# Kernel optimization log

Hardware: AMD Instinct MI355X
Metric: run time of the kernel (lower is better)

## Reference

```python
import jax, jax.numpy as jnp
import numpy as np

L = 4096          # total packed length
HID = 2560        # hidden_size
H = 8             # num_attention_heads
KV = 4            # num_key_value_heads
HD = 256          # head_dim
SW = 1024         # sliding_window
SCALING = 256.0 ** -0.5  # query_pre_attn_scalar ** -0.5
EPS = 1e-6
ROPE_BASE = 10000.0


def setup_inputs() -> dict:
    key = jax.random.key(0)
    ks = jax.random.split(key, 9)
    hidden_states = jax.random.normal(ks[0], (L, HID), jnp.float32)
    Wq = jax.random.normal(ks[1], (HID, H * HD), jnp.float32) * 0.02
    Wk = jax.random.normal(ks[2], (HID, KV * HD), jnp.float32) * 0.02
    Wv = jax.random.normal(ks[3], (HID, KV * HD), jnp.float32) * 0.02
    Wo = jax.random.normal(ks[4], (H * HD, HID), jnp.float32) * 0.02
    q_norm_w = jax.random.normal(ks[5], (HD,), jnp.float32) * 0.1
    k_norm_w = jax.random.normal(ks[6], (HD,), jnp.float32) * 0.1
    # 4 packed sequences of length 1024 each; positions restart per sequence
    cu_seqlens = jnp.array([0, 1024, 2048, 3072, 4096], jnp.int32)
    pos = jnp.tile(jnp.arange(1024, dtype=jnp.float32), 4)  # [L]
    inv_freq = 1.0 / (ROPE_BASE ** (jnp.arange(0, HD, 2, dtype=jnp.float32) / HD))
    freqs = pos[:, None] * inv_freq[None, :]                # [L, HD/2]
    emb = jnp.concatenate([freqs, freqs], axis=-1)          # [L, HD]
    cos, sin = jnp.cos(emb), jnp.sin(emb)
    return {"hidden_states": hidden_states, "cos": cos, "sin": sin,
            "Wq": Wq, "Wk": Wk, "Wv": Wv, "Wo": Wo,
            "q_norm_w": q_norm_w, "k_norm_w": k_norm_w,
            "cu_seqlens": cu_seqlens}


def _rotate_half(x):
    x1, x2 = x[..., : HD // 2], x[..., HD // 2:]
    return jnp.concatenate([-x2, x1], axis=-1)


def _rms_norm(x, w):
    # Gemma3RMSNorm: x * rsqrt(mean(x^2) + eps) * (1 + w)
    x32 = x.astype(jnp.float32)
    out = x32 * jax.lax.rsqrt(jnp.mean(x32 * x32, axis=-1, keepdims=True) + EPS)
    return (out * (1.0 + w.astype(jnp.float32))).astype(x.dtype)


def _packed_sliding_causal_mask(cu_seqlens, total_len):
    pos = jnp.arange(total_len)
    seq_ids = jnp.searchsorted(cu_seqlens[1:], pos, side='right')
    seq_mask = seq_ids[:, None] == seq_ids[None, :]
    dist = pos[None, :] - pos[:, None]                      # pos[j] - pos[i]
    causal = dist <= 0
    window = dist >= -(SW - 1)                              # left_window = SW - 1
    keep = seq_mask & causal & window
    return jnp.where(keep, 0.0, -jnp.inf).astype(jnp.float32)  # [L, L]


def reference(hidden_states, cos, sin, Wq, Wk, Wv, Wo, q_norm_w, k_norm_w, cu_seqlens):
    total_len = hidden_states.shape[0]
    # projections -> [n_heads, L, head_dim]
    q = (hidden_states @ Wq).reshape(total_len, H, HD).transpose(1, 0, 2)
    k = (hidden_states @ Wk).reshape(total_len, KV, HD).transpose(1, 0, 2)
    v = (hidden_states @ Wv).reshape(total_len, KV, HD).transpose(1, 0, 2)
    q = _rms_norm(q, q_norm_w)
    k = _rms_norm(k, k_norm_w)
    # RoPE (cos/sin broadcast over heads)
    q = q * cos + _rotate_half(q) * sin
    k = k * cos + _rotate_half(k) * sin
    # GQA repeat_kv: [KV, L, HD] -> [H, L, HD]
    n_rep = H // KV
    k = jnp.repeat(k, n_rep, axis=0)
    v = jnp.repeat(v, n_rep, axis=0)
    mask = _packed_sliding_causal_mask(cu_seqlens, total_len)
    scores = jnp.einsum('hqd,hkd->hqk', q, k) * SCALING + mask[None]
    attn = jax.nn.softmax(scores.astype(jnp.float32), axis=-1).astype(q.dtype)
    out = jnp.einsum('hqk,hkd->qhd', attn, v).reshape(total_len, H * HD)
    return out @ Wo  # [L, hidden]
```

## Files before the change

kernel.cpp:

```cpp
#include <hip/hip_runtime.h>
#include <hip/hip_bf16.h>

typedef unsigned short u16;
typedef float f32x4 __attribute__((ext_vector_type(4)));
typedef short bf16x8 __attribute__((ext_vector_type(8)));

__device__ __forceinline__ float bf2f(u16 u) {
    union { float f; unsigned int i; } c; c.i = ((unsigned int)u) << 16; return c.f;
}
__device__ __forceinline__ u16 f2bf(float f) {
    union { float f; unsigned int i; } c; c.f = f;
    unsigned int r = c.i + 0x7fffu + ((c.i >> 16) & 1u);
    return (u16)(r >> 16);
}
__device__ __forceinline__ void gload16(const void* g, void* l) {
    __builtin_amdgcn_global_load_lds(
        (const __attribute__((address_space(1))) void*)g,
        (__attribute__((address_space(3))) void*)l, 16, 0, 0);
}

__global__ __launch_bounds__(256) void convert_f32_bf16(
    const float* __restrict__ in, u16* __restrict__ out, int n8)
{
    int i = blockIdx.x * 256 + threadIdx.x;
    if (i >= n8) return;
    const float4 a = *(const float4*)&in[i * 8];
    const float4 b = *(const float4*)&in[i * 8 + 4];
    bf16x8 o;
    o[0] = (short)f2bf(a.x); o[1] = (short)f2bf(a.y);
    o[2] = (short)f2bf(a.z); o[3] = (short)f2bf(a.w);
    o[4] = (short)f2bf(b.x); o[5] = (short)f2bf(b.y);
    o[6] = (short)f2bf(b.z); o[7] = (short)f2bf(b.w);
    *(bf16x8*)&out[i * 8] = o;
}

__global__ __launch_bounds__(256) void transpose_f32_bf16(
    const float* __restrict__ in, u16* __restrict__ out, int R, int C)
{
    __shared__ u16 tile[32][34];
    const int tx = threadIdx.x & 31;
    const int ty = threadIdx.x >> 5;
    const size_t r0 = (size_t)blockIdx.y * 32;
    const size_t c0 = (size_t)blockIdx.x * 32;
#pragma unroll
    for (int i = 0; i < 4; ++i) {
        int r = ty + 8 * i;
        tile[r][tx] = f2bf(in[(r0 + r) * C + c0 + tx]);
    }
    __syncthreads();
#pragma unroll
    for (int i = 0; i < 4; ++i) {
        int r = ty + 8 * i;
        out[(c0 + r) * R + r0 + tx] = tile[tx][r];
    }
}

__global__ __launch_bounds__(256) void transpose_bf16(
    const u16* __restrict__ in, u16* __restrict__ out, int ldin, int ldout)
{
    __shared__ u16 tile[32][34];
    const int tx = threadIdx.x & 31;
    const int ty = threadIdx.x >> 5;
    const size_t r0 = (size_t)blockIdx.y * 32;
    const size_t c0 = (size_t)blockIdx.x * 32;
#pragma unroll
    for (int i = 0; i < 4; ++i) {
        int r = ty + 8 * i;
        tile[r][tx] = in[(r0 + r) * (size_t)ldin + c0 + tx];
    }
    __syncthreads();
#pragma unroll
    for (int i = 0; i < 4; ++i) {
        int r = ty + 8 * i;
        out[(c0 + r) * (size_t)ldout + r0 + tx] = tile[tx][r];
    }
}

template<typename TOUT>
__global__ __launch_bounds__(512, 2) void gemm_bt8p(
    const u16* __restrict__ A, const u16* __restrict__ Bt, TOUT* __restrict__ C,
    int M, int N, int K)
{
    __shared__ u16 As[2][2][128 * 64];
    __shared__ u16 Bs[2][2][128 * 64];
    const int tid  = threadIdx.x;
    const int lane = tid & 63;
    const int w    = tid >> 6;
    const int wm   = w >> 2;
    const int wn   = w & 3;
    const int g    = lane >> 4, c = lane & 15;

    const int nbx = gridDim.x;
    int lin = blockIdx.y * nbx + blockIdx.x;
    const int cpx = (nbx * gridDim.y) >> 3;
    lin = (lin & 7) * cpx + (lin >> 3);
    const size_t mbase = (size_t)(lin / nbx) * 256;
    const size_t nbase = (size_t)(lin % nbx) * 256;

    const int schunk = w * 2;
    const int srow0  = lane >> 3;
    const int sslot  = lane & 7;

    auto stageA = [&](int t, int half) {
        u16* dst = &As[t & 1][half][0];
        const u16* src = A + (mbase + half * 128) * (size_t)K + t * 64;
#pragma unroll
        for (int i = 0; i < 2; ++i) {
            const int ch = schunk + i;
            const int rw = ch * 8 + srow0;
            gload16(src + (size_t)rw * K + ((sslot ^ (rw & 7)) << 3), dst + ch * 512);
        }
    };
    auto stageB = [&](int t, int half) {
        u16* dst = &Bs[t & 1][half][0];
        const u16* src = Bt + (nbase + half * 128) * (size_t)K + t * 64;
#pragma unroll
        for (int i = 0; i < 2; ++i) {
            const int ch = schunk + i;
            const int rw = ch * 8 + srow0;
            gload16(src + (size_t)rw * K + ((sslot ^ (rw & 7)) << 3), dst + ch * 512);
        }
    };
    auto ldA = [&](int t, int m, int kk) -> bf16x8 {
        const int r = m * 16 + c;
        return *(const bf16x8*)&As[t & 1][wm][r * 64 + ((kk * 32 + g * 8) ^ ((r & 7) << 3))];
    };
    auto ldB = [&](int t, int n, int kk) -> bf16x8 {
        const int r = (wn & 1) * 64 + n * 16 + c;
        return *(const bf16x8*)&Bs[t & 1][wn >> 1][r * 64 + ((kk * 32 + g * 8) ^ ((r & 7) << 3))];
    };

    f32x4 acc[8][4];
#pragma unroll
    for (int m = 0; m < 8; ++m)
#pragma unroll
        for (int n = 0; n < 4; ++n) { acc[m][n][0]=0.f; acc[m][n][1]=0.f; acc[m][n][2]=0.f; acc[m][n][3]=0.f; }

    const int nT = K >> 6;

    stageA(0, 0); stageA(0, 1); stageB(0, 0); stageB(0, 1);
    asm volatile("s_waitcnt vmcnt(0)" ::: "memory");
    __builtin_amdgcn_sched_barrier(0);
    __builtin_amdgcn_s_barrier();

    for (int t = 0; t < nT; ++t) {
        bf16x8 bF[4][2], aF[2][2];
        const bool more = (t + 1 < nT);

#pragma unroll
        for (int n = 0; n < 4; ++n) { bF[n][0] = ldB(t, n, 0); bF[n][1] = ldB(t, n, 1); }
#pragma unroll
        for (int i = 0; i < 2; ++i) { aF[i][0] = ldA(t, i, 0); aF[i][1] = ldA(t, i, 1); }
        if (more) { stageA(t + 1, 0); stageA(t + 1, 1); }
        __builtin_amdgcn_s_barrier();
        __builtin_amdgcn_s_setprio(1);
#pragma unroll
        for (int kk = 0; kk < 2; ++kk)
#pragma unroll
            for (int i = 0; i < 2; ++i)
#pragma unroll
                for (int n = 0; n < 4; ++n)
                    acc[i][n] = __builtin_amdgcn_mfma_f32_16x16x32_bf16(
                        aF[i][kk], bF[n][kk], acc[i][n], 0, 0, 0);
        __builtin_amdgcn_s_setprio(0);
        __builtin_amdgcn_s_barrier();

#pragma unroll
        for (int q = 1; q < 4; ++q) {
#pragma unroll
            for (int i = 0; i < 2; ++i) { aF[i][0] = ldA(t, 2*q + i, 0); aF[i][1] = ldA(t, 2*q + i, 1); }
            if (q == 1 && more) { stageB(t + 1, 0); stageB(t + 1, 1); }
            __builtin_amdgcn_s_barrier();
            __builtin_amdgcn_s_setprio(1);
#pragma unroll
            for (int kk = 0; kk < 2; ++kk)
#pragma unroll
                for (int i = 0; i < 2; ++i)
#pragma unroll
                    for (int n = 0; n < 4; ++n)
                        acc[2*q + i][n] = __builtin_amdgcn_mfma_f32_16x16x32_bf16(
                            aF[i][kk], bF[n][kk], acc[2*q + i][n], 0, 0, 0);
            __builtin_amdgcn_s_setprio(0);
            __builtin_amdgcn_s_barrier();
        }

        asm volatile("s_waitcnt vmcnt(0)" ::: "memory");
        __builtin_amdgcn_sched_barrier(0);
        __builtin_amdgcn_s_barrier();
    }

#pragma unroll
    for (int m = 0; m < 8; ++m)
#pragma unroll
        for (int n = 0; n < 4; ++n)
#pragma unroll
            for (int i = 0; i < 4; ++i) {
                size_t r   = mbase + wm * 128 + m * 16 + g * 4 + i;
                size_t col = nbase + wn * 64 + n * 16 + c;
                if constexpr (sizeof(TOUT) == 4) C[r * (size_t)N + col] = acc[m][n][i];
                else                             C[r * (size_t)N + col] = f2bf(acc[m][n][i]);
            }
}

__global__ __launch_bounds__(256) void rmsnorm_rope(
    u16* __restrict__ buf, int ld, const float* __restrict__ wgt,
    const float* __restrict__ cosb, const float* __restrict__ sinb,
    int heads, float outscale)
{
    const int lane = threadIdx.x & 63;
    const int wv   = threadIdx.x >> 6;
    const int rid  = blockIdx.x * 4 + wv;
    const int t    = rid / heads;
    const int h    = rid - t * heads;
    u16* p = buf + (size_t)t * ld + h * 256 + lane * 4;

    ushort4 xu = *(const ushort4*)p;
    float x0 = bf2f(xu.x), x1 = bf2f(xu.y), x2 = bf2f(xu.z), x3 = bf2f(xu.w);
    float ss = x0*x0 + x1*x1 + x2*x2 + x3*x3;
#pragma unroll
    for (int msk = 1; msk < 64; msk <<= 1) ss += __shfl_xor(ss, msk);
    const float rstd = rsqrtf(ss * (1.0f / 256.0f) + 1e-6f);

    const int d0 = lane * 4;
    const float4 wv4 = *(const float4*)&wgt[d0];
    float xn0 = x0 * rstd * (1.0f + wv4.x);
    float xn1 = x1 * rstd * (1.0f + wv4.y);
    float xn2 = x2 * rstd * (1.0f + wv4.z);
    float xn3 = x3 * rstd * (1.0f + wv4.w);

    float pn0 = __shfl_xor(xn0, 32);
    float pn1 = __shfl_xor(xn1, 32);
    float pn2 = __shfl_xor(xn2, 32);
    float pn3 = __shfl_xor(xn3, 32);
    const float sgn = (lane < 32) ? -1.0f : 1.0f;

    const float4 cv = *(const float4*)&cosb[(size_t)t * 256 + d0];
    const float4 sv = *(const float4*)&sinb[(size_t)t * 256 + d0];
    float r0 = (xn0 * cv.x + sgn * pn0 * sv.x) * outscale;
    float r1 = (xn1 * cv.y + sgn * pn1 * sv.y) * outscale;
    float r2 = (xn2 * cv.z + sgn * pn2 * sv.z) * outscale;
    float r3 = (xn3 * cv.w + sgn * pn3 * sv.w) * outscale;

    ushort4 ou;
    ou.x = f2bf(r0); ou.y = f2bf(r1); ou.z = f2bf(r2); ou.w = f2bf(r3);
    *(ushort4*)p = ou;
}

__global__ __launch_bounds__(512, 2) void attn_kernel(
    const u16* __restrict__ q, int ldq,
    const u16* __restrict__ k, int ldk,
    const u16* __restrict__ vT,
    u16* __restrict__ Opart,
    float* __restrict__ stats)
{
    __shared__ u16 Ks[2][32 * 256];
    __shared__ u16 Vs[256 * 40];
    __shared__ u16 P[8][16][56];
    __shared__ float corrsF[8][16];
    const int tid  = threadIdx.x;
    const int lane = tid & 63;
    const int w    = tid >> 6;
    const int g    = lane >> 4, c = lane & 15;
    const int qt   = 15 - blockIdx.x;
    const int s    = blockIdx.y;
    const int kvh  = blockIdx.z & 3;
    const int kvs  = blockIdx.z >> 2;
    const int h    = kvh * 2 + (w >> 2);
    const int seq0 = s << 10;
    const int qrow0 = qt * 64 + (w & 3) * 16;
    const float NEG = -3.0e38f;

    bf16x8 qf[8];
    {
        const u16* qp = q + (size_t)(seq0 + qrow0 + c) * ldq + h * 256 + g * 8;
#pragma unroll
        for (int ch = 0; ch < 8; ++ch) qf[ch] = *(const bf16x8*)(qp + ch * 32);
    }

    const int kchunk0  = w * 2;
    const int krow_in  = (lane >> 5);
    const int kcol_lin = (lane & 31) * 16;
    const u16* kbase = k + (size_t)seq0 * ldk + kvh * 256;
    const int vd  = tid & 255;
    const int vj0 = (tid >> 8) * 2;
    const int vsw = (vd >> 3) & 3;
    const u16* vbase = vT + ((size_t)kvh * 256 + vd) * 4096 + seq0 + vj0 * 8;

    f32x4 oacc[16];
#pragma unroll
    for (int dt = 0; dt < 16; ++dt) { oacc[dt][0]=0.f; oacc[dt][1]=0.f; oacc[dt][2]=0.f; oacc[dt][3]=0.f; }
    float mq = -1e30f;
    float lq = 0.f;

    const int nt = qt + 1;
    const int t0 = kvs * nt;

    bf16x8 vreg[2];
#pragma unroll
    for (int i = 0; i < 2; ++i) {
        const int chunk = kchunk0 + i;
        const int row   = chunk * 2 + krow_in;
        const int bcol  = kcol_lin ^ ((row & 7) << 4);
        gload16(kbase + (size_t)(t0 * 32 + row) * ldk + (bcol >> 1), &Ks[0][chunk * 512]);
    }
#pragma unroll
    for (int j = 0; j < 2; ++j) vreg[j] = *(const bf16x8*)(vbase + t0 * 32 + j * 8);
    __syncthreads();
#pragma unroll
    for (int j = 0; j < 2; ++j)
        *(bf16x8*)&Vs[vd * 40 + (((vj0 + j) ^ vsw) * 8)] = vreg[j];
    __syncthreads();

    for (int ti = 0; ti < nt; ++ti) {
        const int p   = ti & 1;
        const int kv0 = (t0 + ti) * 32;

        if (ti + 1 < nt) {
#pragma unroll
            for (int i = 0; i < 2; ++i) {
                const int chunk = kchunk0 + i;
                const int row   = chunk * 2 + krow_in;
                const int bcol  = kcol_lin ^ ((row & 7) << 4);
                gload16(kbase + (size_t)(kv0 + 32 + row) * ldk + (bcol >> 1),
                        &Ks[p ^ 1][chunk * 512]);
            }
#pragma unroll
            for (int j = 0; j < 2; ++j) vreg[j] = *(const bf16x8*)(vbase + kv0 + 32 + j * 8);
        }

        f32x4 sacc[2];
#pragma unroll
        for (int nh = 0; nh < 2; ++nh) { sacc[nh][0]=0.f; sacc[nh][1]=0.f; sacc[nh][2]=0.f; sacc[nh][3]=0.f; }
        __builtin_amdgcn_s_setprio(1);
#pragma unroll
        for (int nh = 0; nh < 2; ++nh) {
            const int krow = nh * 16 + c;
#pragma unroll
            for (int ch = 0; ch < 8; ++ch) {
                const int sw = ((ch * 64 + g * 16) ^ ((c & 7) << 4)) >> 1;
                bf16x8 kf = *(const bf16x8*)&Ks[p][krow * 256 + sw];
                sacc[nh] = __builtin_amdgcn_mfma_f32_16x16x32_bf16(kf, qf[ch], sacc[nh], 0, 0, 0);
            }
        }
        __builtin_amdgcn_s_setprio(0);

        const int qloc = qrow0 + c;
        float pmax = NEG;
#pragma unroll
        for (int nh = 0; nh < 2; ++nh)
#pragma unroll
            for (int i = 0; i < 4; ++i) {
                if (kv0 + nh * 16 + g * 4 + i > qloc) sacc[nh][i] = NEG;
                pmax = fmaxf(pmax, sacc[nh][i]);
            }
        pmax = fmaxf(pmax, __shfl_xor(pmax, 16));
        pmax = fmaxf(pmax, __shfl_xor(pmax, 32));

        const bool rescale = !__all(pmax - mq <= 8.0f);
        float corr = 1.0f;
        if (rescale) {
            const float mn = fmaxf(mq, pmax);
            corr = __expf(mq - mn);
            mq = mn;
            if (g == 0) corrsF[w][c] = corr;
        }

        float rowsum = 0.f;
        unsigned int pw[4];
#pragma unroll
        for (int nh = 0; nh < 2; ++nh) {
            float p0 = __expf(sacc[nh][0] - mq);
            float p1 = __expf(sacc[nh][1] - mq);
            float p2 = __expf(sacc[nh][2] - mq);
            float p3 = __expf(sacc[nh][3] - mq);
            rowsum += (p0 + p1) + (p2 + p3);
            pw[nh * 2 + 0] = (unsigned int)f2bf(p0) | ((unsigned int)f2bf(p1) << 16);
            pw[nh * 2 + 1] = (unsigned int)f2bf(p2) | ((unsigned int)f2bf(p3) << 16);
        }
#pragma unroll
        for (int nh = 0; nh < 2; ++nh) {
            *(unsigned int*)&P[w][c][nh * 16 + g * 4]     = pw[nh * 2 + 0];
            *(unsigned int*)&P[w][c][nh * 16 + g * 4 + 2] = pw[nh * 2 + 1];
        }
        rowsum += __shfl_xor(rowsum, 16);
        rowsum += __shfl_xor(rowsum, 32);
        lq = lq * corr + rowsum;

        bf16x8 pf = *(const bf16x8*)&P[w][c][g * 8];

        if (rescale) {
            const f32x4 c4 = *(const f32x4*)&corrsF[w][g * 4];
#pragma unroll
            for (int dt = 0; dt < 16; ++dt)
#pragma unroll
                for (int i = 0; i < 4; ++i) oacc[dt][i] *= c4[i];
        }

        __builtin_amdgcn_s_setprio(1);
#pragma unroll
        for (int dt = 0; dt < 16; ++dt) {
            const int d = dt * 16 + c;
            bf16x8 vf = *(const bf16x8*)&Vs[d * 40 + ((g ^ ((d >> 3) & 3)) * 8)];
            oacc[dt] = __builtin_amdgcn_mfma_f32_16x16x32_bf16(pf, vf, oacc[dt], 0, 0, 0);
        }
        __builtin_amdgcn_s_setprio(0);

        __syncthreads();
        if (ti + 1 < nt) {
#pragma unroll
            for (int j = 0; j < 2; ++j)
                *(bf16x8*)&Vs[vd * 40 + (((vj0 + j) ^ vsw) * 8)] = vreg[j];
        }
        __syncthreads();
    }

    u16* op = Opart + (size_t)kvs * 4096 * 2048;
#pragma unroll
    for (int dt = 0; dt < 16; ++dt)
#pragma unroll
        for (int i = 0; i < 4; ++i)
            op[(size_t)(seq0 + qrow0 + g * 4 + i) * 2048 + h * 256 + dt * 16 + c] =
                f2bf(oacc[dt][i]);
    if (g == 0) {
        const int row = seq0 + qrow0 + c;
        stats[(((size_t)kvs * 8 + h) * 2 + 0) * 4096 + row] = mq;
        stats[(((size_t)kvs * 8 + h) * 2 + 1) * 4096 + row] = lq;
    }
}

__global__ __launch_bounds__(256) void merge_partial(
    const u16* __restrict__ Op,
    const float* __restrict__ stats,
    u16* __restrict__ ob)
{
    const int idx = blockIdx.x * 256 + threadIdx.x;
    const int row = idx >> 8;
    const int col = (idx & 255) * 8;
    const int h   = col >> 8;
    const float m0 = stats[((0 * 8 + h) * 2 + 0) * 4096 + row];
    const float l0 = stats[((0 * 8 + h) * 2 + 1) * 4096 + row];
    const float m1 = stats[((1 * 8 + h) * 2 + 0) * 4096 + row];
    const float l1 = stats[((1 * 8 + h) * 2 + 1) * 4096 + row];
    const float mm = fmaxf(m0, m1);
    const float w0 = __expf(m0 - mm);
    const float w1 = __expf(m1 - mm);
    const float inv = 1.0f / (w0 * l0 + w1 * l1);
    const float s0 = w0 * inv, s1 = w1 * inv;
    const size_t base = (size_t)row * 2048 + col;
    bf16x8 a = *(const bf16x8*)&Op[base];
    bf16x8 b = *(const bf16x8*)&Op[(size_t)4096 * 2048 + base];
    bf16x8 r;
#pragma unroll
    for (int j = 0; j < 8; ++j)
        r[j] = (short)f2bf(bf2f((u16)a[j]) * s0 + bf2f((u16)b[j]) * s1);
    *(bf16x8*)&ob[base] = r;
}

extern "C" void kernel_launch(void* const* d_in, const int* in_sizes, int n_in,
                              void* d_out, int out_size, void* d_ws, size_t ws_size,
                              hipStream_t stream)
{
    const float* hid  = (const float*)d_in[0];
    const float* cosb = (const float*)d_in[1];
    const float* sinb = (const float*)d_in[2];
    const float* Wq   = (const float*)d_in[3];
    const float* Wk   = (const float*)d_in[4];
    const float* Wv   = (const float*)d_in[5];
    const float* Wo   = (const float*)d_in[6];
    const float* qnw  = (const float*)d_in[7];
    const float* knw  = (const float*)d_in[8];

    char* ws = (char*)d_ws;
    const size_t R1 = 0;
    const size_t R2 = (size_t)4096 * 2560 * 2;
    const size_t R3 = R2 * 2;
    u16* hidb  = (u16*)(ws + R1);
    u16* WoT   = (u16*)(ws + R1);
    u16* vT    = (u16*)(ws + R1 + (size_t)2560 * 2048 * 2);
    u16* WqkvT = (u16*)(ws + R2);
    u16* ob    = (u16*)(ws + R2);
    u16* qkv   = (u16*)(ws + R3);
    float* stats = (float*)(ws + R3 + (size_t)4096 * 4096 * 2);
    u16* Opart = (u16*)d_out;
    (void)ws_size; (void)in_sizes; (void)n_in; (void)out_size;

    dim3 B(256);
    convert_f32_bf16<<<dim3(4096 * 2560 / 8 / 256), B, 0, stream>>>(hid, hidb, 4096 * 2560 / 8);
    transpose_f32_bf16<<<dim3(2048 / 32, 2560 / 32), B, 0, stream>>>(Wq, WqkvT, 2560, 2048);
    transpose_f32_bf16<<<dim3(1024 / 32, 2560 / 32), B, 0, stream>>>(Wk, WqkvT + (size_t)2048 * 2560, 2560, 1024);
    transpose_f32_bf16<<<dim3(1024 / 32, 2560 / 32), B, 0, stream>>>(Wv, WqkvT + (size_t)3072 * 2560, 2560, 1024);

    gemm_bt8p<u16><<<dim3(16, 16), dim3(512), 0, stream>>>(hidb, WqkvT, qkv, 4096, 4096, 2560);

    transpose_f32_bf16<<<dim3(2560 / 32, 2048 / 32), B, 0, stream>>>(Wo, WoT, 2048, 2560);

    rmsnorm_rope<<<dim3(8192), B, 0, stream>>>(qkv, 4096, qnw, cosb, sinb, 8, 0.0625f);
    rmsnorm_rope<<<dim3(4096), B, 0, stream>>>(qkv + 2048, 4096, knw, cosb, sinb, 4, 1.0f);

    transpose_bf16<<<dim3(1024 / 32, 4096 / 32), B, 0, stream>>>(qkv + 3072, vT, 4096, 4096);

    attn_kernel<<<dim3(16, 4, 8), dim3(512), 0, stream>>>(qkv, 4096, qkv + 2048, 4096, vT,
                                                          Opart, stats);
    merge_partial<<<dim3(4096), B, 0, stream>>>(Opart, stats, ob);

    gemm_bt8p<float><<<dim3(10, 16), dim3(512), 0, stream>>>(ob, WoT, (float*)d_out, 4096, 2560, 2048);
}
```

Measured before the change: 297.5 us.

## Merge prep and post-QKV launches, deepen GEMM load pipelining, rebalance attention order

Folds the hidden-state conversion and all four weight transposes into one prep launch, and fuses the q/k RMSNorm+RoPE with the V transpose into one post-QKV launch. WoT moves to its own workspace region so it can be produced before the QKV GEMM without aliasing. Both changes cut launch count and per-launch tail gaps. The GEMM restages A and B loads in finer groups spread across the four compute phases, with partial vmcnt waits so global loads overlap MFMA work. Attention blocks with a nonzero kvs index now walk query tiles in reverse order, meant to balance causal work across the grid. The finer waits rely on exact counts of outstanding loads, which is fragile if the compiler reorders memory operations.

```diff
diff --git a/kernel.cpp b/kernel.cpp
--- a/kernel.cpp
+++ b/kernel.cpp
@@ -19,29 +19,15 @@
         (__attribute__((address_space(3))) void*)l, 16, 0, 0);
 }
 
-__global__ __launch_bounds__(256) void convert_f32_bf16(
-    const float* __restrict__ in, u16* __restrict__ out, int n8)
-{
-    int i = blockIdx.x * 256 + threadIdx.x;
-    if (i >= n8) return;
-    const float4 a = *(const float4*)&in[i * 8];
-    const float4 b = *(const float4*)&in[i * 8 + 4];
-    bf16x8 o;
-    o[0] = (short)f2bf(a.x); o[1] = (short)f2bf(a.y);
-    o[2] = (short)f2bf(a.z); o[3] = (short)f2bf(a.w);
-    o[4] = (short)f2bf(b.x); o[5] = (short)f2bf(b.y);
-    o[6] = (short)f2bf(b.z); o[7] = (short)f2bf(b.w);
-    *(bf16x8*)&out[i * 8] = o;
-}
-
-__global__ __launch_bounds__(256) void transpose_f32_bf16(
-    const float* __restrict__ in, u16* __restrict__ out, int R, int C)
+__device__ __forceinline__ void dev_tr_f32_bf16(
+    const float* __restrict__ in, u16* __restrict__ out, int R, int C,
+    int bx, int by)
 {
     __shared__ u16 tile[32][34];
     const int tx = threadIdx.x & 31;
     const int ty = threadIdx.x >> 5;
-    const size_t r0 = (size_t)blockIdx.y * 32;
-    const size_t c0 = (size_t)blockIdx.x * 32;
+    const size_t r0 = (size_t)by * 32;
+    const size_t c0 = (size_t)bx * 32;
 #pragma unroll
     for (int i = 0; i < 4; ++i) {
         int r = ty + 8 * i;
@@ -55,24 +41,35 @@
     }
 }
 
-__global__ __launch_bounds__(256) void transpose_bf16(
-    const u16* __restrict__ in, u16* __restrict__ out, int ldin, int ldout)
-{
-    __shared__ u16 tile[32][34];
-    const int tx = threadIdx.x & 31;
-    const int ty = threadIdx.x >> 5;
-    const size_t r0 = (size_t)blockIdx.y * 32;
-    const size_t c0 = (size_t)blockIdx.x * 32;
-#pragma unroll
-    for (int i = 0; i < 4; ++i) {
-        int r = ty + 8 * i;
-        tile[r][tx] = in[(r0 + r) * (size_t)ldin + c0 + tx];
-    }
-    __syncthreads();
-#pragma unroll
-    for (int i = 0; i < 4; ++i) {
-        int r = ty + 8 * i;
-        out[(c0 + r) * (size_t)ldout + r0 + tx] = tile[tx][r];
+__global__ __launch_bounds__(256) void prep_all(
+    const float* __restrict__ hid, u16* __restrict__ hidb,
+    const float* __restrict__ Wq, const float* __restrict__ Wk,
+    const float* __restrict__ Wv, const float* __restrict__ Wo,
+    u16* __restrict__ WqkvT, u16* __restrict__ WoT)
+{
+    const int b = blockIdx.x;
+    if (b < 5120) {
+        int i = b * 256 + threadIdx.x;
+        const float4 a = *(const float4*)&hid[(size_t)i * 8];
+        const float4 v = *(const float4*)&hid[(size_t)i * 8 + 4];
+        bf16x8 o;
+        o[0] = (short)f2bf(a.x); o[1] = (short)f2bf(a.y);
+        o[2] = (short)f2bf(a.z); o[3] = (short)f2bf(a.w);
+        o[4] = (short)f2bf(v.x); o[5] = (short)f2bf(v.y);
+        o[6] = (short)f2bf(v.z); o[7] = (short)f2bf(v.w);
+        *(bf16x8*)&hidb[(size_t)i * 8] = o;
+    } else if (b < 10240) {
+        int id = b - 5120;
+        dev_tr_f32_bf16(Wq, WqkvT, 2560, 2048, id % 64, id / 64);
+    } else if (b < 12800) {
+        int id = b - 10240;
+        dev_tr_f32_bf16(Wk, WqkvT + (size_t)2048 * 2560, 2560, 1024, id % 32, id / 32);
+    } else if (b < 15360) {
+        int id = b - 12800;
+        dev_tr_f32_bf16(Wv, WqkvT + (size_t)3072 * 2560, 2560, 1024, id % 32, id / 32);
+    } else {
+        int id = b - 15360;
+        dev_tr_f32_bf16(Wo, WoT, 2048, 2560, id % 80, id / 80);
     }
 }
 
@@ -97,28 +94,26 @@
     const size_t mbase = (size_t)(lin / nbx) * 256;
     const size_t nbase = (size_t)(lin % nbx) * 256;
 
-    const int schunk = w * 2;
-    const int srow0  = lane >> 3;
-    const int sslot  = lane & 7;
-
-    auto stageA = [&](int t, int half) {
-        u16* dst = &As[t & 1][half][0];
-        const u16* src = A + (mbase + half * 128) * (size_t)K + t * 64;
-#pragma unroll
-        for (int i = 0; i < 2; ++i) {
-            const int ch = schunk + i;
-            const int rw = ch * 8 + srow0;
-            gload16(src + (size_t)rw * K + ((sslot ^ (rw & 7)) << 3), dst + ch * 512);
-        }
+    const int srow0 = lane >> 3;
+    const int sslot = lane & 7;
+    const int swz   = (sslot ^ srow0) << 3;
+
+    auto stageG = [&](int t, int qg) {
+        const int half = w >> 2;
+        const int ch   = qg * 4 + (w & 3);
+        const int rw   = ch * 8 + srow0;
+        gload16(A + (mbase + half * 128 + rw) * (size_t)K + t * 64 + swz,
+                &As[t & 1][half][ch * 512]);
     };
-    auto stageB = [&](int t, int half) {
-        u16* dst = &Bs[t & 1][half][0];
-        const u16* src = Bt + (nbase + half * 128) * (size_t)K + t * 64;
-#pragma unroll
-        for (int i = 0; i < 2; ++i) {
-            const int ch = schunk + i;
-            const int rw = ch * 8 + srow0;
-            gload16(src + (size_t)rw * K + ((sslot ^ (rw & 7)) << 3), dst + ch * 512);
+    auto stageB4 = [&](int t) {
+#pragma unroll
+        for (int i = 0; i < 4; ++i) {
+            const int gc   = w * 4 + i;
+            const int half = gc >> 4;
+            const int ch   = gc & 15;
+            const int rw   = ch * 8 + srow0;
+            gload16(Bt + (nbase + half * 128 + rw) * (size_t)K + t * 64 + swz,
+                    &Bs[t & 1][half][ch * 512]);
         }
     };
     auto ldA = [&](int t, int m, int kk) -> bf16x8 {
@@ -138,8 +133,8 @@
 
     const int nT = K >> 6;
 
-    stageA(0, 0); stageA(0, 1); stageB(0, 0); stageB(0, 1);
-    asm volatile("s_waitcnt vmcnt(0)" ::: "memory");
+    stageG(0, 3); stageB4(0); stageG(0, 0); stageG(0, 1); stageG(0, 2);
+    asm volatile("s_waitcnt vmcnt(2)" ::: "memory");
     __builtin_amdgcn_sched_barrier(0);
     __builtin_amdgcn_s_barrier();
 
@@ -151,7 +146,7 @@
         for (int n = 0; n < 4; ++n) { bF[n][0] = ldB(t, n, 0); bF[n][1] = ldB(t, n, 1); }
 #pragma unroll
         for (int i = 0; i < 2; ++i) { aF[i][0] = ldA(t, i, 0); aF[i][1] = ldA(t, i, 1); }
-        if (more) { stageA(t + 1, 0); stageA(t + 1, 1); }
+        if (more) stageG(t + 1, 3);
         __builtin_amdgcn_s_barrier();
         __builtin_amdgcn_s_setprio(1);
 #pragma unroll
@@ -163,29 +158,64 @@
                     acc[i][n] = __builtin_amdgcn_mfma_f32_16x16x32_bf16(
                         aF[i][kk], bF[n][kk], acc[i][n], 0, 0, 0);
         __builtin_amdgcn_s_setprio(0);
-        __builtin_amdgcn_s_barrier();
-
-#pragma unroll
-        for (int q = 1; q < 4; ++q) {
-#pragma unroll
-            for (int i = 0; i < 2; ++i) { aF[i][0] = ldA(t, 2*q + i, 0); aF[i][1] = ldA(t, 2*q + i, 1); }
-            if (q == 1 && more) { stageB(t + 1, 0); stageB(t + 1, 1); }
-            __builtin_amdgcn_s_barrier();
-            __builtin_amdgcn_s_setprio(1);
-#pragma unroll
-            for (int kk = 0; kk < 2; ++kk)
-#pragma unroll
-                for (int i = 0; i < 2; ++i)
-#pragma unroll
-                    for (int n = 0; n < 4; ++n)
-                        acc[2*q + i][n] = __builtin_amdgcn_mfma_f32_16x16x32_bf16(
-                            aF[i][kk], bF[n][kk], acc[2*q + i][n], 0, 0, 0);
-            __builtin_amdgcn_s_setprio(0);
-            __builtin_amdgcn_s_barrier();
-        }
-
-        asm volatile("s_waitcnt vmcnt(0)" ::: "memory");
+        if (more) asm volatile("s_waitcnt vmcnt(2)" ::: "memory");
+        else      asm volatile("s_waitcnt vmcnt(1)" ::: "memory");
         __builtin_amdgcn_sched_barrier(0);
+        __builtin_amdgcn_s_barrier();
+
+#pragma unroll
+        for (int i = 0; i < 2; ++i) { aF[i][0] = ldA(t, 2 + i, 0); aF[i][1] = ldA(t, 2 + i, 1); }
+        if (more) stageB4(t + 1);
+        __builtin_amdgcn_s_barrier();
+        __builtin_amdgcn_s_setprio(1);
+#pragma unroll
+        for (int kk = 0; kk < 2; ++kk)
+#pragma unroll
+            for (int i = 0; i < 2; ++i)
+#pragma unroll
+                for (int n = 0; n < 4; ++n)
+                    acc[2 + i][n] = __builtin_amdgcn_mfma_f32_16x16x32_bf16(
+                        aF[i][kk], bF[n][kk], acc[2 + i][n], 0, 0, 0);
+        __builtin_amdgcn_s_setprio(0);
+        if (more) asm volatile("s_waitcnt vmcnt(5)" ::: "memory");
+        else      asm volatile("s_waitcnt vmcnt(0)" ::: "memory");
+        __builtin_amdgcn_sched_barrier(0);
+        __builtin_amdgcn_s_barrier();
+
+#pragma unroll
+        for (int i = 0; i < 2; ++i) { aF[i][0] = ldA(t, 4 + i, 0); aF[i][1] = ldA(t, 4 + i, 1); }
+        if (more) stageG(t + 1, 0);
+        __builtin_amdgcn_s_barrier();
+        __builtin_amdgcn_s_setprio(1);
+#pragma unroll
+        for (int kk = 0; kk < 2; ++kk)
+#pragma unroll
+            for (int i = 0; i < 2; ++i)
+#pragma unroll
+                for (int n = 0; n < 4; ++n)
+                    acc[4 + i][n] = __builtin_amdgcn_mfma_f32_16x16x32_bf16(
+                        aF[i][kk], bF[n][kk], acc[4 + i][n], 0, 0, 0);
+        __builtin_amdgcn_s_setprio(0);
+        __builtin_amdgcn_s_barrier();
+
+#pragma unroll
+        for (int i = 0; i < 2; ++i) { aF[i][0] = ldA(t, 6 + i, 0); aF[i][1] = ldA(t, 6 + i, 1); }
+        if (more) { stageG(t + 1, 1); stageG(t + 1, 2); }
+        __builtin_amdgcn_s_barrier();
+        __builtin_amdgcn_s_setprio(1);
+#pragma unroll
+        for (int kk = 0; kk < 2; ++kk)
+#pragma unroll
+            for (int i = 0; i < 2; ++i)
+#pragma unroll
+                for (int n = 0; n < 4; ++n)
+                    acc[6 + i][n] = __builtin_amdgcn_mfma_f32_16x16x32_bf16(
+                        aF[i][kk], bF[n][kk], acc[6 + i][n], 0, 0, 0);
+        __builtin_amdgcn_s_setprio(0);
+        if (more) {
+            asm volatile("s_waitcnt vmcnt(2)" ::: "memory");
+            __builtin_amdgcn_sched_barrier(0);
+        }
         __builtin_amdgcn_s_barrier();
     }
 
@@ -202,14 +232,14 @@
             }
 }
 
-__global__ __launch_bounds__(256) void rmsnorm_rope(
+__device__ __forceinline__ void dev_rmsnorm_rope(
     u16* __restrict__ buf, int ld, const float* __restrict__ wgt,
     const float* __restrict__ cosb, const float* __restrict__ sinb,
-    int heads, float outscale)
+    int heads, float outscale, int blk)
 {
     const int lane = threadIdx.x & 63;
     const int wv   = threadIdx.x >> 6;
-    const int rid  = blockIdx.x * 4 + wv;
+    const int rid  = blk * 4 + wv;
     const int t    = rid / heads;
     const int h    = rid - t * heads;
     u16* p = buf + (size_t)t * ld + h * 256 + lane * 4;
@@ -244,6 +274,39 @@
     ushort4 ou;
     ou.x = f2bf(r0); ou.y = f2bf(r1); ou.z = f2bf(r2); ou.w = f2bf(r3);
     *(ushort4*)p = ou;
+}
+
+__global__ __launch_bounds__(256) void postqkv(
+    u16* __restrict__ qkv, const float* __restrict__ qnw,
+    const float* __restrict__ knw, const float* __restrict__ cosb,
+    const float* __restrict__ sinb, u16* __restrict__ vT)
+{
+    const int b = blockIdx.x;
+    if (b < 8192) {
+        dev_rmsnorm_rope(qkv, 4096, qnw, cosb, sinb, 8, 0.0625f, b);
+    } else if (b < 12288) {
+        dev_rmsnorm_rope(qkv + 2048, 4096, knw, cosb, sinb, 4, 1.0f, b - 8192);
+    } else {
+        __shared__ u16 tile[32][34];
+        const int id = b - 12288;
+        const int bx = id & 31, by = id >> 5;
+        const int tx = threadIdx.x & 31;
+        const int ty = threadIdx.x >> 5;
+        const size_t r0 = (size_t)by * 32;
+        const size_t c0 = (size_t)bx * 32;
+        const u16* in = qkv + 3072;
+#pragma unroll
+        for (int i = 0; i < 4; ++i) {
+            int r = ty + 8 * i;
+            tile[r][tx] = in[(r0 + r) * 4096 + c0 + tx];
+        }
+        __syncthreads();
+#pragma unroll
+        for (int i = 0; i < 4; ++i) {
+            int r = ty + 8 * i;
+            vT[(c0 + r) * 4096 + r0 + tx] = tile[tx][r];
+        }
+    }
 }
 
 __global__ __launch_bounds__(512, 2) void attn_kernel(
@@ -261,10 +324,10 @@
     const int lane = tid & 63;
     const int w    = tid >> 6;
     const int g    = lane >> 4, c = lane & 15;
-    const int qt   = 15 - blockIdx.x;
     const int s    = blockIdx.y;
     const int kvh  = blockIdx.z & 3;
     const int kvs  = blockIdx.z >> 2;
+    const int qt   = kvs ? (int)blockIdx.x : 15 - (int)blockIdx.x;
     const int h    = kvh * 2 + (w >> 2);
     const int seq0 = s << 10;
     const int qrow0 = qt * 64 + (w & 3) * 16;
@@ -481,23 +544,17 @@
     u16* ob    = (u16*)(ws + R2);
     u16* qkv   = (u16*)(ws + R3);
     float* stats = (float*)(ws + R3 + (size_t)4096 * 4096 * 2);
+    u16* WoT2  = (u16*)(ws + R3 + (size_t)4096 * 4096 * 2 + (1 << 20));
     u16* Opart = (u16*)d_out;
     (void)ws_size; (void)in_sizes; (void)n_in; (void)out_size;
+    WoT = WoT2;
 
     dim3 B(256);
-    convert_f32_bf16<<<dim3(4096 * 2560 / 8 / 256), B, 0, stream>>>(hid, hidb, 4096 * 2560 / 8);
-    transpose_f32_bf16<<<dim3(2048 / 32, 2560 / 32), B, 0, stream>>>(Wq, WqkvT, 2560, 2048);
-    transpose_f32_bf16<<<dim3(1024 / 32, 2560 / 32), B, 0, stream>>>(Wk, WqkvT + (size_t)2048 * 2560, 2560, 1024);
-    transpose_f32_bf16<<<dim3(1024 / 32, 2560 / 32), B, 0, stream>>>(Wv, WqkvT + (size_t)3072 * 2560, 2560, 1024);
+    prep_all<<<dim3(20480), B, 0, stream>>>(hid, hidb, Wq, Wk, Wv, Wo, WqkvT, WoT);
 
     gemm_bt8p<u16><<<dim3(16, 16), dim3(512), 0, stream>>>(hidb, WqkvT, qkv, 4096, 4096, 2560);
 
-    transpose_f32_bf16<<<dim3(2560 / 32, 2048 / 32), B, 0, stream>>>(Wo, WoT, 2048, 2560);
-
-    rmsnorm_rope<<<dim3(8192), B, 0, stream>>>(qkv, 4096, qnw, cosb, sinb, 8, 0.0625f);
-    rmsnorm_rope<<<dim3(4096), B, 0, stream>>>(qkv + 2048, 4096, knw, cosb, sinb, 4, 1.0f);
-
-    transpose_bf16<<<dim3(1024 / 32, 4096 / 32), B, 0, stream>>>(qkv + 3072, vT, 4096, 4096);
+    postqkv<<<dim3(16384), B, 0, stream>>>(qkv, qnw, knw, cosb, sinb, vT);
 
     attn_kernel<<<dim3(16, 4, 8), dim3(512), 0, stream>>>(qkv, 4096, qkv + 2048, 4096, vT,
                                                           Opart, stats);
```

Result: faster. 263.9 us (-11.3%).
